# Performance work log

Hardware: AMD Instinct MI355X
Metric: run time of the kernel (lower is better)

## Reference

```python
import jax, jax.numpy as jnp
import numpy as np

T, HID, H = 1024, 2048, 16
LQ, LKV = 1536, 512
DR, DN, DQ, DV = 64, 128, 192, 128
HI, DI, TOPK = 16, 128, 256
EPS = 1e-6
NEG = -1e30


def _rms(x, g, eps=EPS):
    return x * jax.lax.rsqrt(jnp.mean(x * x, -1, keepdims=True) + eps) * g


def _ln(x, w, b, eps=1e-6):
    m = jnp.mean(x, -1, keepdims=True)
    v = jnp.mean((x - m) ** 2, -1, keepdims=True)
    return (x - m) * jax.lax.rsqrt(v + eps) * w + b


def _rope_interleave(x, cos, sin):
    # HF apply_rotary_pos_emb_interleave: de-interleave even/odd then standard rotate_half.
    x1, x2 = x[..., 0::2], x[..., 1::2]
    xr = jnp.concatenate([x1, x2], -1)
    rot = jnp.concatenate([-x2, x1], -1)
    return xr * cos + rot * sin


def _sparse_indices(hidden, q_lat, cos, sin, ks, ke, i_wqb, i_wk, i_ln_w, i_ln_b, i_wproj):
    # hidden [T,HID], q_lat [T,LQ]; returns [T,TOPK] int32 (sentinel index = T)
    t = hidden.shape[0]
    q_idx = (q_lat @ i_wqb.T).reshape(t, HI, DI)
    k_idx = _ln(hidden @ i_wk.T, i_ln_w, i_ln_b)          # [T,DI]
    w = hidden @ i_wproj.T                                 # [T,HI]
    q_pe = _rope_interleave(q_idx[..., :DR], cos[:, None, :], sin[:, None, :])
    k_pe = _rope_interleave(k_idx[..., :DR], cos, sin)
    qi = jnp.concatenate([q_pe, q_idx[..., DR:]], -1)      # [T,HI,DI]
    ki = jnp.concatenate([k_pe, k_idx[..., DR:]], -1)      # [T,DI]
    weight_scale = DI ** -0.5 * HI ** -0.5
    logits = jnp.einsum('thd,sd->ths', qi, ki)             # [T,HI,T]
    score = jnp.einsum('ths,th->ts', jax.nn.relu(logits), w) * weight_scale
    pos = jnp.arange(t)
    valid = (pos[None, :] >= ks[:, None]) & (pos[None, :] <= ke[:, None])
    score = jnp.where(valid, score, NEG)
    vals, idx = jax.lax.top_k(score, TOPK)
    return jnp.where(vals <= NEG / 2, t, idx).astype(jnp.int32)


def reference(hidden_states, cos, sin, ks, ke,
              w_qa, g_qa, w_qb, w_kva, g_kva, w_kvb, w_o,
              i_wqb, i_wk, i_ln_w, i_ln_b, i_wproj):
    t = hidden_states.shape[1]
    # low-rank projections
    q_lat = _rms(hidden_states @ w_qa.T, g_qa)             # [1,T,LQ]
    ckv = hidden_states @ w_kva.T                          # [1,T,LKV+DR]
    k_c = _rms(ckv[..., :LKV], g_kva)                      # [1,T,LKV]
    k_r = _rope_interleave(ckv[..., LKV:], cos[None], sin[None])  # [1,T,DR]
    # fp8 indexer (reference math in fp32), no-grad in original
    indices = _sparse_indices(hidden_states[0], q_lat[0], cos, sin, ks, ke,
                              i_wqb, i_wk, i_ln_w, i_ln_b, i_wproj)  # [T,TOPK]
    # MLA up-proj with weight absorption
    q_full = (q_lat @ w_qb.T).reshape(1, t, H, DQ)
    q_nope, q_rope = q_full[..., :DN], q_full[..., DN:]
    q_rope = _rope_interleave(q_rope, cos[None, :, None, :], sin[None, :, None, :])
    w_b = w_kvb.reshape(H, DN + DV, LKV)
    w_kn, w_v = w_b[:, :DN, :], w_b[:, DN:, :]
    q_abs = jnp.einsum('bshd,hdk->bshk', q_nope, w_kn)     # absorb k_nope up-proj
    sq = jnp.concatenate([q_abs, q_rope], -1)[0]           # [T,H,LKV+DR]
    skv = jnp.concatenate([k_c, k_r], -1)[0]               # [T,LKV+DR]
    skv = jnp.concatenate([skv, jnp.zeros((1, LKV + DR), skv.dtype)], 0)  # sentinel row
    # sparse attention over gathered top-k KV rows
    kv_g = skv[indices]                                    # [T,TOPK,LKV+DR]
    logits = jnp.einsum('thd,tjd->thj', sq, kv_g) * (DQ ** -0.5)
    logits = jnp.where(indices[:, None, :] == t, NEG, logits)
    p = jax.nn.softmax(logits, -1)
    out = jnp.einsum('thj,tjk->thk', p, kv_g[..., :LKV])   # values = compressed kv
    o = jnp.einsum('thk,hdk->thd', out, w_v)               # un-absorb v up-proj
    return o.reshape(1, t, H * DV) @ w_o.T


def setup_inputs() -> dict:
    key = jax.random.key(0)
    k = jax.random.split(key, 12)
    n = lambda kk, shape, s: jax.random.normal(kk, shape, jnp.float32) * s
    pos = jnp.arange(T, dtype=jnp.float32)
    inv = 1.0 / (10000.0 ** (jnp.arange(0, DR, 2, dtype=jnp.float32) / DR))
    ang = pos[:, None] * inv[None, :]
    cos = jnp.concatenate([jnp.cos(ang), jnp.cos(ang)], -1)
    sin = jnp.concatenate([jnp.sin(ang), jnp.sin(ang)], -1)
    return dict(
        hidden_states=n(k[0], (1, T, HID), 1.0),
        cos=cos, sin=sin,
        ks=jnp.zeros((T,), jnp.int32),
        ke=jnp.arange(T, dtype=jnp.int32),  # causal: keys s <= t valid
        w_qa=n(k[1], (LQ, HID), HID ** -0.5),
        g_qa=jnp.ones((LQ,), jnp.float32),
        w_qb=n(k[2], (H * DQ, LQ), LQ ** -0.5),
        w_kva=n(k[3], (LKV + DR, HID), HID ** -0.5),
        g_kva=jnp.ones((LKV,), jnp.float32),
        w_kvb=n(k[4], (H * (DN + DV), LKV), LKV ** -0.5),
        w_o=n(k[5], (HID, H * DV), (H * DV) ** -0.5),
        i_wqb=n(k[6], (HI * DI, LQ), LQ ** -0.5),
        i_wk=n(k[7], (DI, HID), HID ** -0.5),
        i_ln_w=jnp.ones((DI,), jnp.float32),
        i_ln_b=jnp.zeros((DI,), jnp.float32),
        i_wproj=n(k[8], (HI, HID), HID ** -0.5),
    )
```

## Files before the change

kernel.cpp:

```cpp
#include <hip/hip_runtime.h>
#include <hip/hip_bf16.h>
#include <cmath>

#define T_ 1024
#define HID_ 2048
#define H_ 16
#define LQ_ 1536
#define LKV_ 512
#define DR_ 64
#define DN_ 128
#define DQ_ 192
#define DV_ 128
#define HI_ 16
#define DI_ 128
#define TOPK_ 256
#define NEGF (-1e30f)

typedef short bfrag_t __attribute__((ext_vector_type(8)));
typedef float f32x4 __attribute__((ext_vector_type(4)));

__device__ __forceinline__ float wave_sum64(float v) {
#pragma unroll
  for (int off = 32; off; off >>= 1) v += __shfl_xor(v, off);
  return v;
}

#define GLL(g, l) __builtin_amdgcn_global_load_lds((const __attribute__((address_space(1))) void*)(g), \
                                     (__attribute__((address_space(3))) void*)(l), 16, 0, 0)

__global__ __launch_bounds__(256) void zero_k(float4* __restrict__ p, int n4) {
  int i = blockIdx.x * 256 + threadIdx.x;
  if (i < n4) p[i] = make_float4(0.f, 0.f, 0.f, 0.f);
}

template<typename CT>
__global__ __launch_bounds__(256) void gemm_bf_k(
    const short* __restrict__ A, int lda, long long sA,
    const short* __restrict__ B, int ldb, long long sB,
    CT* __restrict__ C, int ldc, long long sC,
    int Nout, int K)
{
  __shared__ short As[2][128 * 32];
  __shared__ short Bs[2][128 * 32];
  A += (long long)blockIdx.z * sA;
  B += (long long)blockIdx.z * sB;
  C += (long long)blockIdx.z * sC;
  const int tid = threadIdx.x;
  const int bm = blockIdx.y * 128, bn = blockIdx.x * 128;
  const int wave = tid >> 6, lane = tid & 63;
  const int wm = (wave >> 1) * 64, wn = (wave & 1) * 64;
  const int sr = tid >> 2;
  const int scol = (tid & 3) * 8;
  const int m0 = lane & 15, koff = (lane >> 4) * 8;
  f32x4 acc[4][4] = {};
  const short* ga = A + (long long)(bm + sr) * lda + scol;
  const short* gb = B + (long long)(bn + sr) * ldb + scol;
#define STAGE_BF(buf, off) \
    GLL(ga + (off), As[buf] + tid * 8); GLL(ga + (off) + 64 * lda, As[buf] + tid * 8 + 2048); \
    GLL(gb + (off), Bs[buf] + tid * 8); GLL(gb + (off) + 64 * ldb, Bs[buf] + tid * 8 + 2048);
  const int niter = K >> 5;
  STAGE_BF(0, 0);
  for (int it = 0; it < niter; ++it) {
    const int cur = it & 1;
    if (it + 1 < niter) {
      STAGE_BF(cur ^ 1, (it + 1) * 32);
      asm volatile("s_waitcnt vmcnt(4)\ns_barrier" ::: "memory");
    } else {
      asm volatile("s_waitcnt vmcnt(0)\ns_barrier" ::: "memory");
    }
    bfrag_t af[4], bfv[4];
#pragma unroll
    for (int i = 0; i < 4; ++i)
      af[i] = *(const bfrag_t*)(As[cur] + (wm + i * 16 + m0) * 32 + koff);
#pragma unroll
    for (int j = 0; j < 4; ++j)
      bfv[j] = *(const bfrag_t*)(Bs[cur] + (wn + j * 16 + m0) * 32 + koff);
#pragma unroll
    for (int i = 0; i < 4; ++i)
#pragma unroll
      for (int j = 0; j < 4; ++j)
        acc[i][j] = __builtin_amdgcn_mfma_f32_16x16x32_bf16(af[i], bfv[j], acc[i][j], 0, 0, 0);
    asm volatile("s_barrier" ::: "memory");
  }
#undef STAGE_BF
  const int cr = (lane >> 4) * 4, cc = lane & 15;
#pragma unroll
  for (int i = 0; i < 4; ++i) {
    int row = bm + wm + i * 16 + cr;
#pragma unroll
    for (int j = 0; j < 4; ++j) {
      int col = bn + wn + j * 16 + cc;
      if (col < Nout) {
#pragma unroll
        for (int r = 0; r < 4; ++r)
          C[(long long)(row + r) * ldc + col] = (CT)(acc[i][j][r]);
      }
    }
  }
}

__global__ __launch_bounds__(256) void gemm_bfs_k(
    const short* __restrict__ A, int lda,
    const short* __restrict__ B, int ldb,
    float* __restrict__ C, int ldc, int Nout, int K)
{
  __shared__ short As[2][128 * 32];
  __shared__ short Bs[2][128 * 32];
  const long long kbase = (long long)blockIdx.z * K;
  const int tid = threadIdx.x;
  const int bm = blockIdx.y * 128, bn = blockIdx.x * 128;
  const int wave = tid >> 6, lane = tid & 63;
  const int wm = (wave >> 1) * 64, wn = (wave & 1) * 64;
  const int sr = tid >> 2;
  const int scol = (tid & 3) * 8;
  const int m0 = lane & 15, koff = (lane >> 4) * 8;
  f32x4 acc[4][4] = {};
  const short* ga = A + (long long)(bm + sr) * lda + kbase + scol;
  const short* gb = B + (long long)(bn + sr) * ldb + kbase + scol;
#define STAGE_BS(buf, off) \
    GLL(ga + (off), As[buf] + tid * 8); GLL(ga + (off) + 64 * lda, As[buf] + tid * 8 + 2048); \
    GLL(gb + (off), Bs[buf] + tid * 8); GLL(gb + (off) + 64 * ldb, Bs[buf] + tid * 8 + 2048);
  const int niter = K >> 5;
  STAGE_BS(0, 0);
  for (int it = 0; it < niter; ++it) {
    const int cur = it & 1;
    if (it + 1 < niter) {
      STAGE_BS(cur ^ 1, (it + 1) * 32);
      asm volatile("s_waitcnt vmcnt(4)\ns_barrier" ::: "memory");
    } else {
      asm volatile("s_waitcnt vmcnt(0)\ns_barrier" ::: "memory");
    }
    bfrag_t af[4], bfv[4];
#pragma unroll
    for (int i = 0; i < 4; ++i)
      af[i] = *(const bfrag_t*)(As[cur] + (wm + i * 16 + m0) * 32 + koff);
#pragma unroll
    for (int j = 0; j < 4; ++j)
      bfv[j] = *(const bfrag_t*)(Bs[cur] + (wn + j * 16 + m0) * 32 + koff);
#pragma unroll
    for (int i = 0; i < 4; ++i)
#pragma unroll
      for (int j = 0; j < 4; ++j)
        acc[i][j] = __builtin_amdgcn_mfma_f32_16x16x32_bf16(af[i], bfv[j], acc[i][j], 0, 0, 0);
    asm volatile("s_barrier" ::: "memory");
  }
#undef STAGE_BS
  const int cr = (lane >> 4) * 4, cc = lane & 15;
#pragma unroll
  for (int i = 0; i < 4; ++i) {
    int row = bm + wm + i * 16 + cr;
#pragma unroll
    for (int j = 0; j < 4; ++j) {
      int col = bn + wn + j * 16 + cc;
      if (col < Nout) {
#pragma unroll
        for (int r = 0; r < 4; ++r)
          atomicAdd(&C[(long long)(row + r) * ldc + col], acc[i][j][r]);
      }
    }
  }
}

__global__ __launch_bounds__(256) void gemm3_k(
    const short* __restrict__ Ah, const short* __restrict__ Al, int lda,
    const short* __restrict__ Bh, const short* __restrict__ Bl, int ldb,
    float* __restrict__ C, int ldc, int Nout, int K)
{
  __shared__ short Ahs[2][128 * 32];
  __shared__ short Als[2][128 * 32];
  __shared__ short Bhs[2][128 * 32];
  __shared__ short Bls[2][128 * 32];
  const long long kbase = (long long)blockIdx.z * K;
  const int tid = threadIdx.x;
  const int bm = blockIdx.y * 128, bn = blockIdx.x * 128;
  const int wave = tid >> 6, lane = tid & 63;
  const int wm = (wave >> 1) * 64, wn = (wave & 1) * 64;
  const int sr = tid >> 2;
  const int scol = (tid & 3) * 8;
  const int m0 = lane & 15, koff = (lane >> 4) * 8;
  f32x4 acc[4][4] = {};
  const short* gah = Ah + (long long)(bm + sr) * lda + kbase + scol;
  const short* gal = Al + (long long)(bm + sr) * lda + kbase + scol;
  const short* gbh = Bh + (long long)(bn + sr) * ldb + kbase + scol;
  const short* gbl = Bl + (long long)(bn + sr) * ldb + kbase + scol;
#define STAGE_3(buf, off) \
    GLL(gah + (off), Ahs[buf] + tid * 8); GLL(gah + (off) + 64 * lda, Ahs[buf] + tid * 8 + 2048); \
    GLL(gal + (off), Als[buf] + tid * 8); GLL(gal + (off) + 64 * lda, Als[buf] + tid * 8 + 2048); \
    GLL(gbh + (off), Bhs[buf] + tid * 8); GLL(gbh + (off) + 64 * ldb, Bhs[buf] + tid * 8 + 2048); \
    GLL(gbl + (off), Bls[buf] + tid * 8); GLL(gbl + (off) + 64 * ldb, Bls[buf] + tid * 8 + 2048);
  const int niter = K >> 5;
  STAGE_3(0, 0);
  for (int it = 0; it < niter; ++it) {
    const int cur = it & 1;
    if (it + 1 < niter) {
      STAGE_3(cur ^ 1, (it + 1) * 32);
      asm volatile("s_waitcnt vmcnt(8)\ns_barrier" ::: "memory");
    } else {
      asm volatile("s_waitcnt vmcnt(0)\ns_barrier" ::: "memory");
    }
    bfrag_t afh[4], afl[4], bfh[4], bfl[4];
#pragma unroll
    for (int i = 0; i < 4; ++i) {
      afh[i] = *(const bfrag_t*)(Ahs[cur] + (wm + i * 16 + m0) * 32 + koff);
      afl[i] = *(const bfrag_t*)(Als[cur] + (wm + i * 16 + m0) * 32 + koff);
    }
#pragma unroll
    for (int j = 0; j < 4; ++j) {
      bfh[j] = *(const bfrag_t*)(Bhs[cur] + (wn + j * 16 + m0) * 32 + koff);
      bfl[j] = *(const bfrag_t*)(Bls[cur] + (wn + j * 16 + m0) * 32 + koff);
    }
#pragma unroll
    for (int i = 0; i < 4; ++i)
#pragma unroll
      for (int j = 0; j < 4; ++j)
        acc[i][j] = __builtin_amdgcn_mfma_f32_16x16x32_bf16(afh[i], bfh[j], acc[i][j], 0, 0, 0);
#pragma unroll
    for (int i = 0; i < 4; ++i)
#pragma unroll
      for (int j = 0; j < 4; ++j)
        acc[i][j] = __builtin_amdgcn_mfma_f32_16x16x32_bf16(afh[i], bfl[j], acc[i][j], 0, 0, 0);
#pragma unroll
    for (int i = 0; i < 4; ++i)
#pragma unroll
      for (int j = 0; j < 4; ++j)
        acc[i][j] = __builtin_amdgcn_mfma_f32_16x16x32_bf16(afl[i], bfh[j], acc[i][j], 0, 0, 0);
    asm volatile("s_barrier" ::: "memory");
  }
#undef STAGE_3
  const int cr = (lane >> 4) * 4, cc = lane & 15;
  const bool spl = (gridDim.z > 1);
#pragma unroll
  for (int i = 0; i < 4; ++i) {
    int row = bm + wm + i * 16 + cr;
#pragma unroll
    for (int j = 0; j < 4; ++j) {
      int col = bn + wn + j * 16 + cc;
      if (col < Nout) {
#pragma unroll
        for (int r = 0; r < 4; ++r) {
          if (spl) atomicAdd(&C[(long long)(row + r) * ldc + col], acc[i][j][r]);
          else     C[(long long)(row + r) * ldc + col] = acc[i][j][r];
        }
      }
    }
  }
}

__global__ __launch_bounds__(256) void cast_bf16_k(const float* __restrict__ src,
                                                   __hip_bfloat16* __restrict__ dst, int n4) {
  int i = blockIdx.x * 256 + threadIdx.x;
  if (i >= n4) return;
  float4 v = ((const float4*)src)[i];
  union { ushort4 u; __hip_bfloat16 h[4]; } o;
  o.h[0] = __float2bfloat16(v.x); o.h[1] = __float2bfloat16(v.y);
  o.h[2] = __float2bfloat16(v.z); o.h[3] = __float2bfloat16(v.w);
  ((ushort4*)dst)[i] = o.u;
}

__global__ __launch_bounds__(256) void decomp_k(const float* __restrict__ src,
                                                __hip_bfloat16* __restrict__ hi,
                                                __hip_bfloat16* __restrict__ lo, int n4) {
  int i = blockIdx.x * 256 + threadIdx.x;
  if (i >= n4) return;
  float4 v = ((const float4*)src)[i];
  float f[4] = {v.x, v.y, v.z, v.w};
  union { ushort4 u; __hip_bfloat16 h[4]; } oh, ol;
#pragma unroll
  for (int j = 0; j < 4; ++j) {
    __hip_bfloat16 h = __float2bfloat16(f[j]);
    oh.h[j] = h;
    ol.h[j] = __float2bfloat16(f[j] - __bfloat162float(h));
  }
  ((ushort4*)hi)[i] = oh.u;
  ((ushort4*)lo)[i] = ol.u;
}

__global__ __launch_bounds__(256) void cast_pad_k(const float* __restrict__ src,
                                                  __hip_bfloat16* __restrict__ dst,
                                                  int N, int K4, int Npad) {
  int i = blockIdx.x * 256 + threadIdx.x;
  if (i >= Npad * K4) return;
  int r = i / K4;
  float4 v = make_float4(0.f, 0.f, 0.f, 0.f);
  if (r < N) v = ((const float4*)src)[i];
  union { ushort4 u; __hip_bfloat16 h[4]; } o;
  o.h[0] = __float2bfloat16(v.x); o.h[1] = __float2bfloat16(v.y);
  o.h[2] = __float2bfloat16(v.z); o.h[3] = __float2bfloat16(v.w);
  ((ushort4*)dst)[i] = o.u;
}

__global__ __launch_bounds__(256) void wkn_t_k(const float* __restrict__ wkvb,
                                               __hip_bfloat16* __restrict__ dst) {
  __shared__ float tile[64][65];
  const int h = blockIdx.z, k0 = blockIdx.y * 64, d0 = blockIdx.x * 64;
  const int c = threadIdx.x & 63, r0 = threadIdx.x >> 6;
#pragma unroll
  for (int rr = 0; rr < 16; ++rr) {
    int r = r0 + rr * 4;
    tile[r][c] = wkvb[((h * 256 + d0 + r) << 9) + k0 + c];
  }
  __syncthreads();
#pragma unroll
  for (int rr = 0; rr < 16; ++rr) {
    int r = r0 + rr * 4;
    dst[((h * 512 + k0 + r) << 7) + d0 + c] = __float2bfloat16(tile[c][r]);
  }
}

__global__ __launch_bounds__(256) void wv_cast_k(const float* __restrict__ wkvb,
                                                 __hip_bfloat16* __restrict__ dst) {
  int i = blockIdx.x * 256 + threadIdx.x;
  int k = i & 511, dv = (i >> 9) & 127, h = i >> 16;
  dst[i] = __float2bfloat16(wkvb[((h * 256 + 128 + dv) << 9) + k]);
}

__global__ __launch_bounds__(256) void rms_inplace_k(float* x, const float* __restrict__ g,
                                                     int C) {
  int t = blockIdx.x, tid = threadIdx.x;
  float* row = x + (long long)t * C;
  float ss = 0.f;
  for (int i = tid; i < C; i += 256) { float v = row[i]; ss += v * v; }
  __shared__ float red[4];
  ss = wave_sum64(ss);
  if ((tid & 63) == 0) red[tid >> 6] = ss;
  __syncthreads();
  float sc = rsqrtf((red[0] + red[1] + red[2] + red[3]) / (float)C + 1e-6f);
  for (int i = tid; i < C; i += 256) row[i] = row[i] * sc * g[i];
}

__global__ __launch_bounds__(256) void skv_build_k(const float* __restrict__ ckv,
                                                   const float* __restrict__ g,
                                                   const float* __restrict__ cosb,
                                                   const float* __restrict__ sinb,
                                                   __hip_bfloat16* __restrict__ skv) {
  int t = blockIdx.x, tid = threadIdx.x;
  __hip_bfloat16* out = skv + (long long)t * 576;
  if (t == T_) { for (int i = tid; i < 576; i += 256) out[i] = __float2bfloat16(0.f); return; }
  const float* row = ckv + (long long)t * 576;
  float ss = 0.f;
  for (int i = tid; i < 512; i += 256) { float v = row[i]; ss += v * v; }
  __shared__ float red[4];
  ss = wave_sum64(ss);
  if ((tid & 63) == 0) red[tid >> 6] = ss;
  __syncthreads();
  float sc = rsqrtf((red[0] + red[1] + red[2] + red[3]) / 512.f + 1e-6f);
  for (int i = tid; i < 512; i += 256) out[i] = __float2bfloat16(row[i] * sc * g[i]);
  if (tid < 64) {
    int j = tid, j2 = tid & 31;
    float c = cosb[t * 64 + j], s = sinb[t * 64 + j];
    float a = row[512 + 2 * j2], b = row[512 + 2 * j2 + 1];
    out[512 + j] = __float2bfloat16((j < 32) ? (a * c - b * s) : (a * s + b * c));
  }
}

__global__ __launch_bounds__(64) void rope_qi_k(float* qi, const float* __restrict__ cosb,
                                                const float* __restrict__ sinb) {
  int b = blockIdx.x, t = b >> 4, j = threadIdx.x, j2 = j & 31;
  float* x = qi + (long long)b * DI_;
  float c = cosb[t * 64 + j], s = sinb[t * 64 + j];
  float a = x[2 * j2], bb = x[2 * j2 + 1];
  float o = (j < 32) ? (a * c - bb * s) : (a * s + bb * c);
  x[j] = o;
}

__global__ __launch_bounds__(128) void ki_ln_rope_k(float* kbuf, const float* __restrict__ w,
                                                    const float* __restrict__ bia,
                                                    const float* __restrict__ cosb,
                                                    const float* __restrict__ sinb) {
  int t = blockIdx.x, i = threadIdx.x;
  float* row = kbuf + (long long)t * DI_;
  float x = row[i];
  __shared__ float red[2];
  float s1 = wave_sum64(x);
  if ((i & 63) == 0) red[i >> 6] = s1;
  __syncthreads();
  float mean = (red[0] + red[1]) / 128.f;
  float d = x - mean;
  __syncthreads();
  float s2 = wave_sum64(d * d);
  if ((i & 63) == 0) red[i >> 6] = s2;
  __syncthreads();
  float var = (red[0] + red[1]) / 128.f;
  float y = d * rsqrtf(var + 1e-6f) * w[i] + bia[i];
  __shared__ float rowl[128];
  rowl[i] = y;
  __syncthreads();
  float outv = y;
  if (i < 64) {
    int j2 = i & 31;
    float c = cosb[t * 64 + i], s = sinb[t * 64 + i];
    float a = rowl[2 * j2], b = rowl[2 * j2 + 1];
    outv = (i < 32) ? (a * c - b * s) : (a * s + b * c);
  }
  row[i] = outv;
}

__global__ __launch_bounds__(64) void rope_q_sq_k(const __hip_bfloat16* __restrict__ qfull,
                                                  const float* __restrict__ cosb,
                                                  const float* __restrict__ sinb,
                                                  __hip_bfloat16* __restrict__ sq) {
  int b = blockIdx.x, t = b >> 4, h = b & 15, j = threadIdx.x, j2 = j & 31;
  const __hip_bfloat16* x = qfull + (long long)t * 3072 + h * 192 + 128;
  float c = cosb[t * 64 + j], s = sinb[t * 64 + j];
  float a = __bfloat162float(x[2 * j2]), bb = __bfloat162float(x[2 * j2 + 1]);
  float o = (j < 32) ? (a * c - bb * s) : (a * s + bb * c);
  sq[((long long)t * H_ + h) * 576 + 512 + j] = __float2bfloat16(o);
}

__global__ __launch_bounds__(256) void wproj_k(const float* __restrict__ hidden,
                                               const float* __restrict__ wp,
                                               float* __restrict__ out) {
  int wave = threadIdx.x >> 6, lane = threadIdx.x & 63;
  int t = blockIdx.x * 4 + wave;
  const float4* x4 = (const float4*)(hidden + (long long)t * 2048);
  float acc[16] = {};
  for (int c = lane; c < 512; c += 64) {
    float4 xv = x4[c];
#pragma unroll
    for (int h = 0; h < 16; ++h) {
      float4 wv = ((const float4*)(wp + h * 2048))[c];
      acc[h] += xv.x * wv.x + xv.y * wv.y + xv.z * wv.z + xv.w * wv.w;
    }
  }
#pragma unroll
  for (int h = 0; h < 16; ++h) {
    float s = wave_sum64(acc[h]);
    if (lane == 0) out[t * 16 + h] = s;
  }
}

__global__ __launch_bounds__(256) void score_topk_k(
    const short* __restrict__ qi_hi, const short* __restrict__ qi_lo,
    const short* __restrict__ ki_hi, const short* __restrict__ ki_lo,
    const float* __restrict__ wproj, const int* __restrict__ ks,
    const int* __restrict__ ke, int* __restrict__ indices)
{
  __shared__ float s_score[T_];
  __shared__ unsigned s_key[T_];
  __shared__ unsigned s_hist[256];
  __shared__ float s_w[HI_];
  __shared__ unsigned s_wsum[4];
  __shared__ unsigned s_binsel[2];
  __shared__ unsigned s_cnt;
  const int t = blockIdx.x, tid = threadIdx.x;
  const int wave = tid >> 6, lane = tid & 63;
  const int m0 = lane & 15, quad = lane >> 4;
  if (tid < HI_) s_w[tid] = wproj[t * HI_ + tid] * 0.022097086912079608f;
  if (tid == 0) s_cnt = 0;
  __syncthreads();

  bfrag_t ah[4], al[4];
  {
    const short* qh = qi_hi + ((long long)t * HI_ + m0) * DI_ + quad * 8;
    const short* ql = qi_lo + ((long long)t * HI_ + m0) * DI_ + quad * 8;
#pragma unroll
    for (int k = 0; k < 4; ++k) {
      ah[k] = *(const bfrag_t*)(qh + k * 32);
      al[k] = *(const bfrag_t*)(ql + k * 32);
    }
  }
  const int lo = ks[t], hi = ke[t];
  for (int tt = 0; tt < 16; ++tt) {
    const int n0 = wave * 256 + tt * 16;
    const short* kh = ki_hi + (n0 + m0) * DI_ + quad * 8;
    const short* kl = ki_lo + (n0 + m0) * DI_ + quad * 8;
    f32x4 acc = {0.f, 0.f, 0.f, 0.f};
#pragma unroll
    for (int k = 0; k < 4; ++k) {
      bfrag_t bh = *(const bfrag_t*)(kh + k * 32);
      bfrag_t bl = *(const bfrag_t*)(kl + k * 32);
      acc = __builtin_amdgcn_mfma_f32_16x16x32_bf16(ah[k], bh, acc, 0, 0, 0);
      acc = __builtin_amdgcn_mfma_f32_16x16x32_bf16(ah[k], bl, acc, 0, 0, 0);
      acc = __builtin_amdgcn_mfma_f32_16x16x32_bf16(al[k], bh, acc, 0, 0, 0);
    }
    float sc = 0.f;
#pragma unroll
    for (int r = 0; r < 4; ++r) sc += fmaxf(acc[r], 0.f) * s_w[quad * 4 + r];
    sc += __shfl_xor(sc, 16);
    sc += __shfl_xor(sc, 32);
    if (quad == 0) {
      int key = n0 + m0;
      s_score[key] = (key >= lo && key <= hi) ? sc : NEGF;
    }
  }
  __syncthreads();

  const int i0 = tid * 4;
#pragma unroll
  for (int j = 0; j < 4; ++j) {
    unsigned u = __float_as_uint(s_score[i0 + j]);
    s_key[i0 + j] = (u & 0x80000000u) ? ~u : (u | 0x80000000u);
  }
  __syncthreads();

  unsigned prefix = 0, Gprev = 0;
  for (int lvl = 0; lvl < 4; ++lvl) {
    const int shift = 24 - 8 * lvl;
    s_hist[tid] = 0;
    __syncthreads();
#pragma unroll
    for (int j = 0; j < 4; ++j) {
      unsigned k = s_key[i0 + j];
      if (lvl == 0 || (k >> (shift + 8)) == prefix)
        atomicAdd(&s_hist[(k >> shift) & 255u], 1u);
    }
    __syncthreads();
    unsigned h = s_hist[255 - tid];
    unsigned sc_ = h;
    for (int off = 1; off < 64; off <<= 1) {
      unsigned v = __shfl_up(sc_, off);
      if (lane >= off) sc_ += v;
    }
    if (lane == 63) s_wsum[wave] = sc_;
    __syncthreads();
    unsigned wo = 0;
    for (int w = 0; w < wave; ++w) wo += s_wsum[w];
    unsigned incl = sc_ + wo, excl = incl - h;
    unsigned Rn = 256 - Gprev;
    if (excl < Rn && Rn <= incl) { s_binsel[0] = 255 - (unsigned)tid; s_binsel[1] = excl; }
    __syncthreads();
    prefix = (prefix << 8) | s_binsel[0];
    Gprev += s_binsel[1];
  }
  const unsigned thr = prefix;
  const unsigned Rq = 256 - Gprev;
  const unsigned negfkey = ~__float_as_uint(NEGF);

  unsigned eqc = 0;
#pragma unroll
  for (int j = 0; j < 4; ++j) eqc += (s_key[i0 + j] == thr) ? 1u : 0u;
  unsigned esc = eqc;
  for (int off = 1; off < 64; off <<= 1) {
    unsigned v = __shfl_up(esc, off);
    if (lane >= off) esc += v;
  }
  if (lane == 63) s_wsum[wave] = esc;
  __syncthreads();
  unsigned eo = 0;
  for (int w = 0; w < wave; ++w) eo += s_wsum[w];
  unsigned rank = esc + eo - eqc;

#pragma unroll
  for (int j = 0; j < 4; ++j) {
    unsigned k = s_key[i0 + j];
    int outv = (k == negfkey) ? T_ : (i0 + j);
    if (k > thr) {
      unsigned slot = atomicAdd(&s_cnt, 1u);
      indices[t * TOPK_ + slot] = outv;
    } else if (k == thr) {
      if (rank < Rq) indices[t * TOPK_ + Gprev + rank] = outv;
      rank++;
    }
  }
}

#define SP_LD 257
#define PB_LD 264
#define VT_LD 258
__global__ __launch_bounds__(256) void attn_k(
    const short* __restrict__ sq, const short* __restrict__ skv,
    const int* __restrict__ indices, __hip_bfloat16* __restrict__ attn_out)
{
  __shared__ int s_ind[TOPK_];
  __shared__ __align__(16) char s_un[64 * PB_LD * 2];
  float* s_p  = (float*)s_un;
  short* s_pb = (short*)(s_un + 16448);
  short* s_vt = (short*)s_un;
  const int t = blockIdx.x, tid = threadIdx.x;
  const int wave = tid >> 6, lane = tid & 63;
  const int m0 = lane & 15, quad = lane >> 4;
  s_ind[tid] = indices[t * TOPK_ + tid];
  __syncthreads();

  {
    const int jb = wave * 64;
    int rows[4];
    const short* kvp[4];
#pragma unroll
    for (int j = 0; j < 4; ++j) {
      rows[j] = s_ind[jb + j * 16 + m0];
      kvp[j] = skv + rows[j] * 576 + quad * 8;
    }
    const short* qp = sq + ((long long)t * H_ + m0) * 576 + quad * 8;
    f32x4 qacc[4] = {};
    for (int ks = 0; ks < 18; ++ks) {
      const int k0 = ks * 32;
      bfrag_t aq = *(const bfrag_t*)(qp + k0);
#pragma unroll
      for (int j = 0; j < 4; ++j) {
        bfrag_t bq = *(const bfrag_t*)(kvp[j] + k0);
        qacc[j] = __builtin_amdgcn_mfma_f32_16x16x32_bf16(aq, bq, qacc[j], 0, 0, 0);
      }
    }
    const float scale = 0.07216878364870322f;
#pragma unroll
    for (int j = 0; j < 4; ++j) {
      int key = jb + j * 16 + m0;
      bool msk = (rows[j] == T_);
#pragma unroll
      for (int r = 0; r < 4; ++r)
        s_p[(quad * 4 + r) * SP_LD + key] = msk ? NEGF : qacc[j][r] * scale;
    }
  }
  __syncthreads();

  for (int h = wave * 4; h < wave * 4 + 4; ++h) {
    float* ph = s_p + h * SP_LD;
    float m = -3.4e38f;
    for (int j = lane; j < TOPK_; j += 64) m = fmaxf(m, ph[j]);
#pragma unroll
    for (int off = 32; off; off >>= 1) m = fmaxf(m, __shfl_xor(m, off));
    float sum = 0.f;
    for (int j = lane; j < TOPK_; j += 64) {
      float e = __expf(ph[j] - m);
      ph[j] = e; sum += e;
    }
    sum = wave_sum64(sum);
    float inv = 1.f / sum;
    for (int j = lane; j < TOPK_; j += 64) ph[j] *= inv;
  }
  __syncthreads();

#pragma unroll
  for (int h = 0; h < H_; ++h)
    s_pb[h * PB_LD + tid] = (short)__bfloat16_as_ushort(__float2bfloat16(s_p[h * SP_LD + tid]));
  __syncthreads();

  bfrag_t apf[8];
#pragma unroll
  for (int kk = 0; kk < 8; ++kk)
    apf[kk] = *(const bfrag_t*)(s_pb + m0 * PB_LD + kk * 32 + quad * 8);

  const int r8 = tid >> 3;
  const int bb = tid & 7;
  int prow[8];
#pragma unroll
  for (int rep = 0; rep < 8; ++rep) prow[rep] = s_ind[r8 + 32 * rep];

  for (int c = 0; c < 8; ++c) {
    __syncthreads();
#pragma unroll
    for (int rep = 0; rep < 8; ++rep) {
      bfrag_t v = *(const bfrag_t*)(skv + (long long)prow[rep] * 576 + c * 64 + bb * 8);
      const int kv = r8 + 32 * rep;
#pragma unroll
      for (int j = 0; j < 8; ++j)
        s_vt[(bb * 8 + j) * VT_LD + kv] = v[j];
    }
    __syncthreads();
    const short* vb = s_vt + (wave * 16 + m0) * VT_LD + quad * 8;
    f32x4 oacc = {0.f, 0.f, 0.f, 0.f};
#pragma unroll
    for (int kk = 0; kk < 8; ++kk) {
      bfrag_t bv = *(const bfrag_t*)(vb + kk * 32);
      oacc = __builtin_amdgcn_mfma_f32_16x16x32_bf16(apf[kk], bv, oacc, 0, 0, 0);
    }
    const int col = c * 64 + wave * 16 + m0;
#pragma unroll
    for (int r = 0; r < 4; ++r)
      attn_out[((long long)t * H_ + quad * 4 + r) * 512 + col] = __float2bfloat16(oacc[r]);
  }
}

extern "C" void kernel_launch(void* const* d_in, const int* in_sizes, int n_in,
                              void* d_out, int out_size, void* d_ws, size_t ws_size,
                              hipStream_t stream) {
  const float* hidden  = (const float*)d_in[0];
  const float* cosb    = (const float*)d_in[1];
  const float* sinb    = (const float*)d_in[2];
  const int*   ks      = (const int*)d_in[3];
  const int*   ke      = (const int*)d_in[4];
  const float* w_qa    = (const float*)d_in[5];
  const float* g_qa    = (const float*)d_in[6];
  const float* w_qb    = (const float*)d_in[7];
  const float* w_kva   = (const float*)d_in[8];
  const float* g_kva   = (const float*)d_in[9];
  const float* w_kvb   = (const float*)d_in[10];
  const float* w_o     = (const float*)d_in[11];
  const float* i_wqb   = (const float*)d_in[12];
  const float* i_wk    = (const float*)d_in[13];
  const float* i_ln_w  = (const float*)d_in[14];
  const float* i_ln_b  = (const float*)d_in[15];
  const float* i_wproj = (const float*)d_in[16];
  float* out = (float*)d_out;
  (void)in_sizes; (void)n_in; (void)out_size; (void)ws_size;

  char* ws = (char*)d_ws;
  __hip_bfloat16* hid_hi  = (__hip_bfloat16*)(ws + 0);
  __hip_bfloat16* hid_lo  = (__hip_bfloat16*)(ws + 4194304);
  float*          q_lat   = (float*)(ws + 8388608);
  __hip_bfloat16* qi_hi   = (__hip_bfloat16*)(ws + 8388608);
  __hip_bfloat16* qlat_hi = (__hip_bfloat16*)(ws + 14680064);
  __hip_bfloat16* qlat_lo = (__hip_bfloat16*)(ws + 17825792);
  float*          qi      = (float*)(ws + 20971520);
  float*          kib     = (float*)(ws + 29360128);
  float*          wbuf    = (float*)(ws + 29884416);
  float*          ckv     = (float*)(ws + 29949952);
  __hip_bfloat16* qi_lo   = (__hip_bfloat16*)(ws + 29949952);
  __hip_bfloat16* ki_hi   = (__hip_bfloat16*)(ws + 34144256);
  __hip_bfloat16* ki_lo   = (__hip_bfloat16*)(ws + 34406400);
  __hip_bfloat16* sq_bf   = (__hip_bfloat16*)(ws + 0);
  __hip_bfloat16* o_bf    = (__hip_bfloat16*)(ws + 0);
  __hip_bfloat16* W       = (__hip_bfloat16*)(ws + 37748736);
  __hip_bfloat16* skv_bf  = (__hip_bfloat16*)(ws + 47185920);
  int*            idxb    = (int*)(ws + 48366720);
  __hip_bfloat16* E       = (__hip_bfloat16*)(ws + 49415296);

  dim3 blk(256);
  const short* Ws = (const short*)W;
  const short* Es = (const short*)E;

  decomp_k<<<2048, blk, 0, stream>>>(hidden, hid_hi, hid_lo, 524288);

  decomp_k<<<3072, blk, 0, stream>>>(w_qa, W, E, 786432);
  zero_k<<<1536, blk, 0, stream>>>((float4*)q_lat, 393216);
  gemm3_k<<<dim3(12, 8, 4), blk, 0, stream>>>(
      (const short*)hid_hi, (const short*)hid_lo, HID_, Ws, Es, HID_, q_lat, LQ_, LQ_, 512);
  rms_inplace_k<<<T_, blk, 0, stream>>>(q_lat, g_qa, LQ_);

  cast_pad_k<<<1280, blk, 0, stream>>>(w_kva, W, 576, 512, 640);
  zero_k<<<576, blk, 0, stream>>>((float4*)ckv, 147456);
  gemm_bfs_k<<<dim3(5, 8, 4), blk, 0, stream>>>(
      (const short*)hid_hi, HID_, Ws, HID_, ckv, 576, 576, 512);
  skv_build_k<<<T_ + 1, blk, 0, stream>>>(ckv, g_kva, cosb, sinb, skv_bf);

  decomp_k<<<1536, blk, 0, stream>>>(q_lat, qlat_hi, qlat_lo, 393216);

  decomp_k<<<3072, blk, 0, stream>>>(i_wqb, W, E, 786432);
  zero_k<<<2048, blk, 0, stream>>>((float4*)qi, 524288);
  gemm3_k<<<dim3(16, 8, 4), blk, 0, stream>>>(
      (const short*)qlat_hi, (const short*)qlat_lo, LQ_, Ws, Es, LQ_, qi, HI_ * DI_, HI_ * DI_, 384);
  rope_qi_k<<<T_ * HI_, dim3(64), 0, stream>>>(qi, cosb, sinb);
  decomp_k<<<2048, blk, 0, stream>>>(qi, qi_hi, qi_lo, 524288);

  decomp_k<<<256, blk, 0, stream>>>(i_wk, W, E, 65536);
  zero_k<<<128, blk, 0, stream>>>((float4*)kib, 32768);
  gemm3_k<<<dim3(1, 8, 8), blk, 0, stream>>>(
      (const short*)hid_hi, (const short*)hid_lo, HID_, Ws, Es, HID_, kib, DI_, DI_, 256);
  ki_ln_rope_k<<<T_, dim3(128), 0, stream>>>(kib, i_ln_w, i_ln_b, cosb, sinb);
  decomp_k<<<128, blk, 0, stream>>>(kib, ki_hi, ki_lo, 32768);

  wproj_k<<<256, blk, 0, stream>>>(hidden, i_wproj, wbuf);

  score_topk_k<<<T_, blk, 0, stream>>>(
      (const short*)qi_hi, (const short*)qi_lo, (const short*)ki_hi, (const short*)ki_lo,
      wbuf, ks, ke, idxb);

  cast_bf16_k<<<4608, blk, 0, stream>>>(w_qb, W, 1179648);
  gemm_bf_k<__hip_bfloat16><<<dim3(24, 8, 1), blk, 0, stream>>>(
      (const short*)qlat_hi, LQ_, 0, Ws, LQ_, 0, (__hip_bfloat16*)E, H_ * DQ_, 0, H_ * DQ_, LQ_);
  rope_q_sq_k<<<T_ * H_, dim3(64), 0, stream>>>(E, cosb, sinb, sq_bf);

  wkn_t_k<<<dim3(2, 8, 16), blk, 0, stream>>>(w_kvb, W);
  gemm_bf_k<__hip_bfloat16><<<dim3(4, 8, 16), blk, 0, stream>>>(
      Es, H_ * DQ_, 192, Ws, DI_, 65536, sq_bf, H_ * 576, 576, LKV_, DN_);

  attn_k<<<T_, blk, 0, stream>>>((const short*)sq_bf, (const short*)skv_bf, idxb, E);

  wv_cast_k<<<4096, blk, 0, stream>>>(w_kvb, W);
  gemm_bf_k<__hip_bfloat16><<<dim3(1, 8, 16), blk, 0, stream>>>(
      Es, H_ * LKV_, 512, Ws, LKV_, 65536, o_bf, H_ * DV_, 128, DV_, LKV_);

  cast_bf16_k<<<4096, blk, 0, stream>>>(w_o, W, 1048576);
  zero_k<<<2048, blk, 0, stream>>>((float4*)out, 524288);
  gemm_bfs_k<<<dim3(16, 8, 4), blk, 0, stream>>>(
      (const short*)o_bf, H_ * DV_, Ws, H_ * DV_, out, HID_, HID_, 512);
}
```

Measured before the change: 588.7 us.

## Double attention block to 512 threads with two V-tile groups and swizzled LDS

The sparse attention kernel now runs 512 threads per token. The QK and softmax work is split across eight waves, and the 64-column V chunks are processed by two independent wave groups, each with its own transposed LDS buffer. The V transpose layout uses an XOR swizzle with a padded stride to reduce LDS bank conflicts, and row indices are read from LDS instead of being cached in registers. Separately, the indexer key GEMM split-K is doubled to add more blocks. The larger LDS footprint and bigger blocks may reduce occupancy.

```diff
diff --git a/kernel.cpp b/kernel.cpp
--- a/kernel.cpp
+++ b/kernel.cpp
@@ -556,45 +556,45 @@
 
 #define SP_LD 257
 #define PB_LD 264
-#define VT_LD 258
-__global__ __launch_bounds__(256) void attn_k(
+#define VT_LD 264
+__global__ __launch_bounds__(512) void attn_k(
     const short* __restrict__ sq, const short* __restrict__ skv,
     const int* __restrict__ indices, __hip_bfloat16* __restrict__ attn_out)
 {
   __shared__ int s_ind[TOPK_];
-  __shared__ __align__(16) char s_un[64 * PB_LD * 2];
+  __shared__ __align__(16) char s_un[2 * 64 * VT_LD * 2];
   float* s_p  = (float*)s_un;
   short* s_pb = (short*)(s_un + 16448);
   short* s_vt = (short*)s_un;
   const int t = blockIdx.x, tid = threadIdx.x;
   const int wave = tid >> 6, lane = tid & 63;
   const int m0 = lane & 15, quad = lane >> 4;
-  s_ind[tid] = indices[t * TOPK_ + tid];
+  if (tid < TOPK_) s_ind[tid] = indices[t * TOPK_ + tid];
   __syncthreads();
 
   {
-    const int jb = wave * 64;
-    int rows[4];
-    const short* kvp[4];
-#pragma unroll
-    for (int j = 0; j < 4; ++j) {
+    const int jb = wave * 32;
+    int rows[2];
+    const short* kvp[2];
+#pragma unroll
+    for (int j = 0; j < 2; ++j) {
       rows[j] = s_ind[jb + j * 16 + m0];
       kvp[j] = skv + rows[j] * 576 + quad * 8;
     }
     const short* qp = sq + ((long long)t * H_ + m0) * 576 + quad * 8;
-    f32x4 qacc[4] = {};
+    f32x4 qacc[2] = {};
     for (int ks = 0; ks < 18; ++ks) {
       const int k0 = ks * 32;
       bfrag_t aq = *(const bfrag_t*)(qp + k0);
 #pragma unroll
-      for (int j = 0; j < 4; ++j) {
+      for (int j = 0; j < 2; ++j) {
         bfrag_t bq = *(const bfrag_t*)(kvp[j] + k0);
         qacc[j] = __builtin_amdgcn_mfma_f32_16x16x32_bf16(aq, bq, qacc[j], 0, 0, 0);
       }
     }
     const float scale = 0.07216878364870322f;
 #pragma unroll
-    for (int j = 0; j < 4; ++j) {
+    for (int j = 0; j < 2; ++j) {
       int key = jb + j * 16 + m0;
       bool msk = (rows[j] == T_);
 #pragma unroll
@@ -604,7 +604,7 @@
   }
   __syncthreads();
 
-  for (int h = wave * 4; h < wave * 4 + 4; ++h) {
+  for (int h = wave * 2; h < wave * 2 + 2; ++h) {
     float* ph = s_p + h * SP_LD;
     float m = -3.4e38f;
     for (int j = lane; j < TOPK_; j += 64) m = fmaxf(m, ph[j]);
@@ -621,9 +621,15 @@
   }
   __syncthreads();
 
-#pragma unroll
-  for (int h = 0; h < H_; ++h)
-    s_pb[h * PB_LD + tid] = (short)__bfloat16_as_ushort(__float2bfloat16(s_p[h * SP_LD + tid]));
+  {
+    const int col = tid & 255, h0 = tid >> 8;
+#pragma unroll
+    for (int h = 0; h < 8; ++h) {
+      const int hh = h0 + h * 2;
+      s_pb[hh * PB_LD + col] =
+          (short)__bfloat16_as_ushort(__float2bfloat16(s_p[hh * SP_LD + col]));
+    }
+  }
   __syncthreads();
 
   bfrag_t apf[8];
@@ -631,31 +637,35 @@
   for (int kk = 0; kk < 8; ++kk)
     apf[kk] = *(const bfrag_t*)(s_pb + m0 * PB_LD + kk * 32 + quad * 8);
 
-  const int r8 = tid >> 3;
+  const int grp = wave >> 2, gw = wave & 3;
+  short* svt = s_vt + grp * (64 * VT_LD);
+  const int r8 = (tid >> 3) & 31;
   const int bb = tid & 7;
-  int prow[8];
-#pragma unroll
-  for (int rep = 0; rep < 8; ++rep) prow[rep] = s_ind[r8 + 32 * rep];
-
-  for (int c = 0; c < 8; ++c) {
+
+  for (int cc = 0; cc < 4; ++cc) {
+    const int c = grp * 4 + cc;
     __syncthreads();
 #pragma unroll
     for (int rep = 0; rep < 8; ++rep) {
-      bfrag_t v = *(const bfrag_t*)(skv + (long long)prow[rep] * 576 + c * 64 + bb * 8);
       const int kv = r8 + 32 * rep;
+      const int row = s_ind[kv];
+      bfrag_t v = *(const bfrag_t*)(skv + (long long)row * 576 + c * 64 + bb * 8);
+      const int colx = kv ^ (bb << 3);
 #pragma unroll
       for (int j = 0; j < 8; ++j)
-        s_vt[(bb * 8 + j) * VT_LD + kv] = v[j];
+        svt[(bb * 8 + j) * VT_LD + colx] = v[j];
     }
     __syncthreads();
-    const short* vb = s_vt + (wave * 16 + m0) * VT_LD + quad * 8;
+    const int d = gw * 16 + m0;
+    const short* vrow = svt + d * VT_LD;
+    const int sx = (d >> 3) << 3;
     f32x4 oacc = {0.f, 0.f, 0.f, 0.f};
 #pragma unroll
     for (int kk = 0; kk < 8; ++kk) {
-      bfrag_t bv = *(const bfrag_t*)(vb + kk * 32);
+      bfrag_t bv = *(const bfrag_t*)(vrow + ((kk * 32 + quad * 8) ^ sx));
       oacc = __builtin_amdgcn_mfma_f32_16x16x32_bf16(apf[kk], bv, oacc, 0, 0, 0);
     }
-    const int col = c * 64 + wave * 16 + m0;
+    const int col = c * 64 + d;
 #pragma unroll
     for (int r = 0; r < 4; ++r)
       attn_out[((long long)t * H_ + quad * 4 + r) * 512 + col] = __float2bfloat16(oacc[r]);
@@ -735,8 +745,8 @@
 
   decomp_k<<<256, blk, 0, stream>>>(i_wk, W, E, 65536);
   zero_k<<<128, blk, 0, stream>>>((float4*)kib, 32768);
-  gemm3_k<<<dim3(1, 8, 8), blk, 0, stream>>>(
-      (const short*)hid_hi, (const short*)hid_lo, HID_, Ws, Es, HID_, kib, DI_, DI_, 256);
+  gemm3_k<<<dim3(1, 8, 16), blk, 0, stream>>>(
+      (const short*)hid_hi, (const short*)hid_lo, HID_, Ws, Es, HID_, kib, DI_, DI_, 128);
   ki_ln_rope_k<<<T_, dim3(128), 0, stream>>>(kib, i_ln_w, i_ln_b, cosb, sinb);
   decomp_k<<<128, blk, 0, stream>>>(kib, ki_hi, ki_lo, 32768);
 
@@ -755,7 +765,7 @@
   gemm_bf_k<__hip_bfloat16><<<dim3(4, 8, 16), blk, 0, stream>>>(
       Es, H_ * DQ_, 192, Ws, DI_, 65536, sq_bf, H_ * 576, 576, LKV_, DN_);
 
-  attn_k<<<T_, blk, 0, stream>>>((const short*)sq_bf, (const short*)skv_bf, idxb, E);
+  attn_k<<<T_, dim3(512), 0, stream>>>((const short*)sq_bf, (const short*)skv_bf, idxb, E);
 
   wv_cast_k<<<4096, blk, 0, stream>>>(w_kvb, W);
   gemm_bf_k<__hip_bfloat16><<<dim3(1, 8, 16), blk, 0, stream>>>(
```

Result: no change. 581.7 us (-1.2%).
